# Optimization experiments

Hardware: AMD Instinct MI355X
Metric: run time of the kernel (lower is better)

Reference implementation:

```python
import jax, jax.numpy as jnp
import numpy as np

D = 300   # hidden dim (Linear(300,300))
L = 160   # seq len, forced by W3 = Linear(160,1)


def _linear(x, W, b):
    # torch Linear: x @ W.T + b, W is (out, in)
    return jnp.matmul(x, W.T) + b


def setup_inputs() -> dict:
    key = jax.random.key(0)
    ks = jax.random.split(key, 16)
    B = 1024
    s = 1.0 / np.sqrt(D)
    inp = {
        'T_feature': jax.random.normal(ks[0], (B, L, D), jnp.float32),
        'CD_feature': jax.random.normal(ks[1], (B, L, D), jnp.float32),
        'Wproj': jax.random.normal(ks[2], (D, D), jnp.float32) * s,
        'bproj': jnp.zeros((D,), jnp.float32),
        'WqT_w': jax.random.normal(ks[3], (D, D), jnp.float32) * s,
        'WqT_b': jnp.zeros((D,), jnp.float32),
        'WqCD_w': jax.random.normal(ks[4], (D, D), jnp.float32) * s,
        'WqCD_b': jnp.zeros((D,), jnp.float32),
        'WkT_w': jax.random.normal(ks[5], (D, D), jnp.float32) * s,
        'WkT_b': jnp.zeros((D,), jnp.float32),
        'WkCD_w': jax.random.normal(ks[6], (D, D), jnp.float32) * s,
        'WkCD_b': jnp.zeros((D,), jnp.float32),
        'W3_w': jax.random.normal(ks[7], (1, L), jnp.float32) * (1.0 / np.sqrt(L)),
        'W3_b': jnp.zeros((1,), jnp.float32),
    }
    return inp


def reference(T_feature, CD_feature, Wproj, bproj, WqT_w, WqT_b, WqCD_w, WqCD_b,
              WkT_w, WkT_b, WkCD_w, WkCD_b, W3_w, W3_b):
    sqrt_d = jnp.sqrt(jnp.float32(D))
    proj_T = _linear(T_feature, Wproj, bproj)     # (B, L, D)
    proj_CD = _linear(CD_feature, Wproj, bproj)   # (B, L, D)

    # N_tensor @ proj_T is just the mean over tokens (weights 1/Len)
    mean_T = jnp.mean(proj_T, axis=1, keepdims=True)          # (B, 1, D)
    qT = _linear(mean_T, WqT_w, WqT_b)                        # (B, 1, D)
    kT = _linear(proj_T, WkT_w, WkT_b)                        # (B, L, D)
    alphaT = jnp.einsum('bqd,bkd->bqk', qT, kT) / sqrt_d      # (B, 1, L)
    ZT = jax.nn.sigmoid(alphaT)

    qCD = _linear(proj_CD, WqCD_w, WqCD_b)                    # (B, L, D)
    kCD = _linear(proj_CD, WkCD_w, WkCD_b)                    # (B, L, D)
    alphaCD = jnp.einsum('bqd,bkd->bqk', qCD, kCD) / sqrt_d   # (B, L, L)
    ZCD = jax.nn.sigmoid(alphaCD)

    # The per-token loop+cat is a plain broadcast multiply: Mt[:,i,:] = ZCD[:,i,:] * ZT[:,0,:]
    Mt = ZCD * ZT                                             # (B, L, L)
    alpha_f = jax.nn.softmax(_linear(Mt, W3_w, W3_b), axis=1) # (B, L, 1)

    # Second loop is a per-token scalar scale: HCD[:,i,:] = alpha_f[:,i,0] * proj_CD[:,i,:]
    HCD = alpha_f * proj_CD                                   # (B, L, D)
    return (proj_T, HCD)
```

## Files before the change

### kernel.cpp

```cpp
#include <hip/hip_runtime.h>
#include <hip/hip_bf16.h>


typedef __attribute__((ext_vector_type(8))) short short8;
typedef __attribute__((ext_vector_type(4))) float f32x4;

#define DP 320

__device__ __forceinline__ unsigned short f2bf(float x) {
  unsigned int u = __builtin_bit_cast(unsigned int, x);
  u += 0x7FFFu + ((u >> 16) & 1u);
  return (unsigned short)(u >> 16);
}
__device__ __forceinline__ float bf2f(unsigned short h) {
  unsigned int u = ((unsigned int)h) << 16;
  return __builtin_bit_cast(float, u);
}
__device__ __forceinline__ void gload16(const void* g, void* l) {
  __builtin_amdgcn_global_load_lds(
      (const __attribute__((address_space(1))) unsigned int*)g,
      (__attribute__((address_space(3))) unsigned int*)l, 16, 0, 0);
}
__device__ __forceinline__ float sigm(float x) { return 1.0f / (1.0f + __expf(-x)); }
__device__ __forceinline__ int swzc(int r, int c) {
  return (c & ~63) | ((((c >> 3) & 7) ^ (r & 7)) << 3) | (c & 7);
}

__global__ __launch_bounds__(320)
void prep1_k(const float* __restrict__ W,
             const float* __restrict__ WqCD_w, const float* __restrict__ WqCD_b,
             const float* __restrict__ WkCD_w, const float* __restrict__ WkCD_b,
             const float* __restrict__ WqT_w, const float* __restrict__ WqT_b,
             const float* __restrict__ WkT_w, const float* __restrict__ WkT_b,
             unsigned short* __restrict__ Wb, float* __restrict__ Wt,
             unsigned short* __restrict__ MaugT, float* __restrict__ Maug_f,
             float* __restrict__ Pmat, float isd) {
  const int x = blockIdx.x, c = threadIdx.x;
  if (x < 320) {
    const int n = x;
    unsigned short v = (n < 300 && c < 300) ? f2bf(W[n * 300 + c]) : (unsigned short)0;
    Wb[n * DP + swzc(n, c)] = v;
    if (n < 300 && c < 300) Wt[c * 304 + n] = W[n * 300 + c];
  } else if (x < 640) {
    const int n = x - 320;
    float v = 0.f;
    if (n <= 300 && c <= 300) {
      for (int o = 0; o < 300; ++o) {
        float a = (c < 300) ? WqCD_w[o * 300 + c] : WqCD_b[o];
        float b = (n < 300) ? WkCD_w[o * 300 + n] : WkCD_b[o];
        v += a * b;
      }
      v *= isd;
    }
    MaugT[n * DP + swzc(n, c)] = f2bf(v);
    Maug_f[n * DP + c] = v;
  } else {
    const int n = x - 640;
    float v = 0.f;
    if (n <= 300 && c <= 300) {
      for (int o = 0; o < 300; ++o) {
        float a = (c < 300) ? WkT_w[o * 300 + c] : WkT_b[o];
        float b = (n < 300) ? WqT_w[o * 300 + n] : WqT_b[o];
        v += a * b;
      }
      v *= isd;
    }
    Pmat[n * DP + c] = v;
  }
}

__global__ __launch_bounds__(320)
void gh_k(const float* __restrict__ Maug_f, const float* __restrict__ W,
          const float* __restrict__ bproj, unsigned short* __restrict__ Gswz,
          float* __restrict__ h) {
  const int n = blockIdx.x, o = threadIdx.x;
  float v = 0.f;
  if (o < 300) {
    for (int c = 0; c < 300; ++c) v += Maug_f[n * DP + c] * W[c * 300 + o];
  } else if (o == 300) {
    float s = 0.f;
    for (int c = 0; c < 300; ++c) s += Maug_f[n * DP + c] * bproj[c];
    h[n] = s + Maug_f[n * DP + 300];
  }
  Gswz[n * DP + swzc(n, o)] = (o < 300) ? f2bf(v) : (unsigned short)0;
}

__global__ __launch_bounds__(256)
void cvt_k(const float* __restrict__ T, const float* __restrict__ CD,
           unsigned short* __restrict__ Abf) {
  unsigned idx = blockIdx.x * 256 + threadIdx.x;
  if (idx >= 327680u * 40u) return;
  unsigned row = idx / 40u, G = idx - row * 40u;
  int kc = G >> 3, sg = G & 7;
  int col0 = kc * 64 + ((sg ^ ((int)row & 7)) << 3);
  const float* base = (row < 163840u) ? T + (size_t)row * 300
                                      : CD + (size_t)(row - 163840u) * 300;
  short8 h;
  if (col0 + 8 <= 300) {
    f32x4 x0 = *(const f32x4*)(base + col0), x1 = *(const f32x4*)(base + col0 + 4);
#pragma unroll
    for (int j = 0; j < 4; ++j) { h[j] = (short)f2bf(x0[j]); h[j + 4] = (short)f2bf(x1[j]); }
  } else {
#pragma unroll
    for (int j = 0; j < 8; ++j) {
      int c = col0 + j;
      h[j] = (short)((c < 300) ? f2bf(base[c]) : (unsigned short)0);
    }
  }
  *(short8*)(Abf + (size_t)row * DP + G * 8) = h;
}

__global__ __launch_bounds__(512)
void gemm_k(const unsigned short* __restrict__ A0, const unsigned short* __restrict__ A1,
            const unsigned short* __restrict__ A2,
            const unsigned short* __restrict__ B01, const unsigned short* __restrict__ B2,
            const float* __restrict__ bias, const float* __restrict__ ybias,
            float* __restrict__ Of, unsigned short* __restrict__ pCDout,
            unsigned short* __restrict__ Yout, int mode_base) {
  __shared__ __align__(16) unsigned short As[2][256 * 64];
  __shared__ __align__(16) unsigned short Bs[2][320 * 64];
  const int tid = threadIdx.x, wid = tid >> 6, lane = tid & 63;
  const int lr = lane & 15, hi = lane >> 4;
  const int mode = mode_base + blockIdx.y;
  const unsigned short* __restrict__ A = (mode == 0) ? A0 : (mode == 1) ? A1 : A2;
  const unsigned short* __restrict__ Bm = (mode == 2) ? B2 : B01;
  const size_t m0 = (size_t)blockIdx.x * 256;

  f32x4 acc[4][10];
#pragma unroll
  for (int i = 0; i < 4; ++i)
#pragma unroll
    for (int j = 0; j < 10; ++j) acc[i][j] = (f32x4){0.f, 0.f, 0.f, 0.f};

  auto stageA = [&](int buf, int kc) {
#pragma unroll
    for (int it = 0; it < 4; ++it) {
      int idx = it * 512 + tid;
      int row = idx >> 3, g = idx & 7;
      gload16(A + (m0 + row) * DP + kc * 64 + g * 8, (char*)As[buf] + idx * 16);
    }
  };
  auto stageB = [&](int buf, int kc) {
#pragma unroll
    for (int it = 0; it < 5; ++it) {
      int idx = it * 512 + tid;
      int row = idx >> 3, g = idx & 7;
      gload16(Bm + (size_t)row * DP + kc * 64 + g * 8, (char*)Bs[buf] + idx * 16);
    }
  };

  stageA(0, 0); stageB(0, 0);
  __syncthreads();
  int buf = 0;
  const int rm = (wid >> 1) * 64, cn = (wid & 1) * 160;
  for (int kc = 0; kc < 5; ++kc) {
    if (kc < 4) { stageA(buf ^ 1, kc + 1); stageB(buf ^ 1, kc + 1); }
#pragma unroll
    for (int kk = 0; kk < 2; ++kk) {
      const int slot = ((kk * 4 + hi) ^ lr) & 7;
      short8 a[4];
#pragma unroll
      for (int mf = 0; mf < 4; ++mf)
        a[mf] = *(const short8*)((const char*)As[buf] + (rm + mf * 16 + lr) * 128 + slot * 16);
#pragma unroll
      for (int nh = 0; nh < 2; ++nh) {
        short8 b[5];
#pragma unroll
        for (int nf = 0; nf < 5; ++nf)
          b[nf] = *(const short8*)((const char*)Bs[buf] +
                                   (cn + (nh * 5 + nf) * 16 + lr) * 128 + slot * 16);
#pragma unroll
        for (int mf = 0; mf < 4; ++mf)
#pragma unroll
          for (int nf = 0; nf < 5; ++nf)
            acc[mf][nh * 5 + nf] =
                __builtin_amdgcn_mfma_f32_16x16x32_bf16(a[mf], b[nf], acc[mf][nh * 5 + nf], 0, 0, 0);
      }
    }
    __syncthreads();
    buf ^= 1;
  }

#pragma unroll
  for (int mf = 0; mf < 4; ++mf)
#pragma unroll
    for (int nf = 0; nf < 10; ++nf) {
      const int col = cn + nf * 16 + lr;
      float bv;
      if (mode == 2) bv = ybias ? ybias[col] : 0.f;
      else bv = (col < 300) ? bias[col] : 0.f;
#pragma unroll
      for (int r = 0; r < 4; ++r) {
        const size_t row = m0 + rm + mf * 16 + hi * 4 + r;
        float v = acc[mf][nf][r] + bv;
        if (mode == 0) {
          if (col < 300) Of[row * 300 + col] = v;
        } else {
          unsigned short u = (mode == 2) ? f2bf(v)
                           : (col < 300) ? f2bf(v)
                           : (col == 300) ? f2bf(1.0f) : (unsigned short)0;
          unsigned short* dst = (mode == 1) ? pCDout : Yout;
          dst[row * DP + swzc((int)row, col)] = u;
        }
      }
    }
}

__global__ __launch_bounds__(320)
void gate2_k(const unsigned short* __restrict__ AbfT, const float* __restrict__ Pmat,
             const float* __restrict__ W, const float* __restrict__ Wt,
             const float* __restrict__ bproj, float* __restrict__ ZT) {
  __shared__ float part[8][320];
  __shared__ float ml[320];
  __shared__ float maug[304];
  __shared__ float vv[304];
  __shared__ float wt[320];
  __shared__ float cpr;
  const int b = blockIdx.x, t = threadIdx.x;
  const int wid = t >> 6, lane = t & 63;
  const size_t sbase = (size_t)b * 160 * DP;
  {
    const int og = t % 40, seg = t / 40;
    float a8[8] = {0.f, 0.f, 0.f, 0.f, 0.f, 0.f, 0.f, 0.f};
    for (int l = seg * 20; l < seg * 20 + 20; ++l) {
      int sg = (og & ~7) | ((og & 7) ^ (l & 7));
      short8 v = *(const short8*)(AbfT + sbase + (size_t)l * DP + sg * 8);
#pragma unroll
      for (int j = 0; j < 8; ++j) a8[j] += bf2f((unsigned short)v[j]);
    }
#pragma unroll
    for (int j = 0; j < 8; ++j) part[seg][og * 8 + j] = a8[j];
  }
  __syncthreads();
  {
    float s = 0.f;
#pragma unroll
    for (int sg = 0; sg < 8; ++sg) s += part[sg][t];
    ml[t] = s * (1.0f / 160.0f);
  }
  __syncthreads();
  if (t < 304) {
    if (t < 300) {
      float s = 0.f;
      for (int o = 0; o < 300; ++o) s += Wt[o * 304 + t] * ml[o];
      maug[t] = s + bproj[t];
    } else maug[t] = (t == 300) ? 1.f : 0.f;
  }
  __syncthreads();
  if (t < 304) {
    float s = 0.f;
    if (t <= 300) for (int a = 0; a <= 300; ++a) s += Pmat[a * DP + t] * maug[a];
    vv[t] = s;
  }
  __syncthreads();
  if (t < 320) {
    if (t < 300) {
      float s = 0.f;
      for (int c = 0; c < 300; ++c) s += vv[c] * W[c * 300 + t];
      wt[t] = s;
    } else {
      wt[t] = 0.f;
      if (t == 300) {
        float s = 0.f;
        for (int c = 0; c < 300; ++c) s += vv[c] * bproj[c];
        cpr = s + vv[300];
      }
    }
  }
  __syncthreads();
  for (int j = wid * 32; j < wid * 32 + 32; ++j) {
    float s = 0.f;
    if (lane < 40) {
      int sg = (lane & ~7) | ((lane & 7) ^ (j & 7));
      short8 v = *(const short8*)(AbfT + sbase + (size_t)j * DP + sg * 8);
#pragma unroll
      for (int k = 0; k < 8; ++k) s += bf2f((unsigned short)v[k]) * wt[lane * 8 + k];
    }
#pragma unroll
    for (int m = 1; m < 64; m <<= 1) s += __shfl_xor(s, m, 64);
    if (lane == 0) ZT[b * 160 + j] = sigm(s + cpr);
  }
}

__global__ __launch_bounds__(320)
void finale_k(const unsigned short* __restrict__ Yg, const unsigned short* __restrict__ Pg,
              const float* __restrict__ ZT, const float* __restrict__ W3w,
              float* __restrict__ out) {
  __shared__ __align__(16) unsigned short Ps[160 * DP];
  __shared__ __align__(16) unsigned short Ys[2][160 * 64];
  __shared__ float t_arr[160];
  __shared__ float s_arr[160];
  __shared__ float red0;
  const int b = blockIdx.x, tid = threadIdx.x, wid = tid >> 6, lane = tid & 63;
  const int lr = lane & 15, hi = lane >> 4;
  const unsigned short* Pb = Pg + (size_t)b * 160 * DP;
  const unsigned short* Yb = Yg + (size_t)b * 160 * DP;

  if (tid < 160) t_arr[tid] = ZT[b * 160 + tid] * W3w[tid];

#pragma unroll
  for (int it = 0; it < 20; ++it) {
    int idx = it * 320 + tid;
    gload16(Pb + (size_t)idx * 8, (char*)Ps + idx * 16);
  }
  auto stageY = [&](int buf, int kc) {
#pragma unroll
    for (int it = 0; it < 4; ++it) {
      int idx = it * 320 + tid;
      int row = idx >> 3, g = idx & 7;
      gload16(Yb + (size_t)row * DP + kc * 64 + g * 8, (char*)Ys[buf] + idx * 16);
    }
  };

  f32x4 acc[2][10];
#pragma unroll
  for (int i = 0; i < 2; ++i)
#pragma unroll
    for (int j = 0; j < 10; ++j) acc[i][j] = (f32x4){0.f, 0.f, 0.f, 0.f};

  stageY(0, 0);
  __syncthreads();
  int buf = 0;
  const int rm = wid * 32;
  for (int kc = 0; kc < 5; ++kc) {
    if (kc < 4) stageY(buf ^ 1, kc + 1);
#pragma unroll
    for (int kk = 0; kk < 2; ++kk) {
      const int slot = ((kk * 4 + hi) ^ lr) & 7;
      short8 a[2], bb[10];
#pragma unroll
      for (int mf = 0; mf < 2; ++mf)
        a[mf] = *(const short8*)((const char*)Ys[buf] + (rm + mf * 16 + lr) * 128 + slot * 16);
#pragma unroll
      for (int nf = 0; nf < 10; ++nf)
        bb[nf] = *(const short8*)((const char*)Ps + (nf * 16 + lr) * 640 + (kc * 8 + slot) * 16);
#pragma unroll
      for (int mf = 0; mf < 2; ++mf)
#pragma unroll
        for (int nf = 0; nf < 10; ++nf)
          acc[mf][nf] = __builtin_amdgcn_mfma_f32_16x16x32_bf16(a[mf], bb[nf], acc[mf][nf], 0, 0, 0);
    }
    __syncthreads();
    buf ^= 1;
  }

  float pp[2][4];
#pragma unroll
  for (int mf = 0; mf < 2; ++mf)
#pragma unroll
    for (int r = 0; r < 4; ++r) {
      float s = 0.f;
#pragma unroll
      for (int nf = 0; nf < 10; ++nf) s += sigm(acc[mf][nf][r]) * t_arr[nf * 16 + lr];
      pp[mf][r] = s;
    }
#pragma unroll
  for (int m = 1; m < 16; m <<= 1)
#pragma unroll
    for (int mf = 0; mf < 2; ++mf)
#pragma unroll
      for (int r = 0; r < 4; ++r) pp[mf][r] += __shfl_xor(pp[mf][r], m, 64);
  if (lr == 0) {
#pragma unroll
    for (int mf = 0; mf < 2; ++mf)
#pragma unroll
      for (int r = 0; r < 4; ++r)
        s_arr[rm + mf * 16 + hi * 4 + r] = pp[mf][r];
  }
  __syncthreads();
  if (wid == 0) {
    float v0 = s_arr[lane], v1 = s_arr[lane + 64];
    float v2 = (lane < 32) ? s_arr[lane + 128] : -3.0e38f;
    float mx = fmaxf(fmaxf(v0, v1), v2);
#pragma unroll
    for (int m = 1; m < 64; m <<= 1) mx = fmaxf(mx, __shfl_xor(mx, m, 64));
    float e0 = __expf(v0 - mx), e1 = __expf(v1 - mx);
    float e2 = (lane < 32) ? __expf(v2 - mx) : 0.f;
    s_arr[lane] = e0; s_arr[lane + 64] = e1;
    if (lane < 32) s_arr[lane + 128] = e2;
    float sm = e0 + e1 + e2;
#pragma unroll
    for (int m = 1; m < 64; m <<= 1) sm += __shfl_xor(sm, m, 64);
    if (lane == 0) red0 = 1.0f / sm;
  }
  __syncthreads();
  const float inv = red0;
  float* ob = out + (size_t)b * 48000;
#pragma unroll 2
  for (int it = 0; it < 19; ++it) {
    int idx = it * 320 + tid;
    if (idx < 6080) {
      int i = idx / 38, cg = idx - i * 38;
      int sg = (cg & ~7) | ((cg & 7) ^ (i & 7));
      short8 pv = *(const short8*)((const char*)Ps + i * 640 + sg * 16);
      float sc = s_arr[i] * inv;
      int c0 = cg * 8;
#pragma unroll
      for (int j = 0; j < 8; ++j) {
        int c = c0 + j;
        if (c < 300) ob[(size_t)i * 300 + c] = sc * bf2f((unsigned short)pv[j]);
      }
    }
  }
}

extern "C" void kernel_launch(void* const* d_in, const int* in_sizes, int n_in,
                              void* d_out, int out_size, void* d_ws, size_t ws_size,
                              hipStream_t stream) {
  (void)in_sizes; (void)n_in; (void)out_size;
  const float* T      = (const float*)d_in[0];
  const float* CD     = (const float*)d_in[1];
  const float* Wproj  = (const float*)d_in[2];
  const float* bproj  = (const float*)d_in[3];
  const float* WqT_w  = (const float*)d_in[4];
  const float* WqT_b  = (const float*)d_in[5];
  const float* WqCD_w = (const float*)d_in[6];
  const float* WqCD_b = (const float*)d_in[7];
  const float* WkT_w  = (const float*)d_in[8];
  const float* WkT_b  = (const float*)d_in[9];
  const float* WkCD_w = (const float*)d_in[10];
  const float* WkCD_b = (const float*)d_in[11];
  const float* W3_w   = (const float*)d_in[12];

  char* ws = (char*)d_ws;
  size_t off = 0;
  auto alloc = [&](size_t bytes) { void* p = ws + off; off = (off + bytes + 255) & ~(size_t)255; return p; };
  unsigned short* Wb     = (unsigned short*)alloc((size_t)DP * DP * 2);
  unsigned short* MaugT  = (unsigned short*)alloc((size_t)DP * DP * 2);
  unsigned short* Gswz   = (unsigned short*)alloc((size_t)DP * DP * 2);
  float* Maug_f = (float*)alloc((size_t)DP * DP * 4);
  float* Pmat   = (float*)alloc((size_t)DP * DP * 4);
  float* Wt     = (float*)alloc((size_t)304 * 304 * 4);
  float* hb     = (float*)alloc((size_t)DP * 4);
  float* ZT     = (float*)alloc((size_t)1024 * 160 * 4);
  unsigned short* Abf = (unsigned short*)alloc((size_t)327680 * DP * 2);
  unsigned short* AbfCD = Abf + (size_t)163840 * DP;

  const size_t half = (size_t)163840 * DP * 2;
  const bool big = (ws_size > off) && ((ws_size - off) >= 2 * half + 1024);
  unsigned short* pCDg = big ? (unsigned short*)alloc(half) : AbfCD;
  unsigned short* Yg   = big ? (unsigned short*)alloc(half) : Abf;

  float* projT = (float*)d_out;
  float* HCD   = (float*)d_out + (size_t)49152000;

  const float isd = 1.0f / sqrtf(300.0f);

  prep1_k<<<dim3(960), dim3(320), 0, stream>>>(Wproj, WqCD_w, WqCD_b, WkCD_w, WkCD_b,
                                               WqT_w, WqT_b, WkT_w, WkT_b,
                                               Wb, Wt, MaugT, Maug_f, Pmat, isd);
  if (big)
    gh_k<<<dim3(320), dim3(320), 0, stream>>>(Maug_f, Wproj, bproj, Gswz, hb);
  cvt_k<<<dim3(51200), dim3(256), 0, stream>>>(T, CD, Abf);

  if (big) {
    gemm_k<<<dim3(640, 3), dim3(512), 0, stream>>>(Abf, AbfCD, AbfCD, Wb, Gswz,
                                                   bproj, hb, projT, pCDg, Yg, 0);
    gate2_k<<<dim3(1024), dim3(320), 0, stream>>>(Abf, Pmat, Wproj, Wt, bproj, ZT);
    finale_k<<<dim3(1024), dim3(320), 0, stream>>>(Yg, pCDg, ZT, W3_w, HCD);
  } else {
    gemm_k<<<dim3(640, 2), dim3(512), 0, stream>>>(Abf, AbfCD, nullptr, Wb, nullptr,
                                                   bproj, nullptr, projT, pCDg, nullptr, 0);
    gate2_k<<<dim3(1024), dim3(320), 0, stream>>>(Abf, Pmat, Wproj, Wt, bproj, ZT);
    gemm_k<<<dim3(640, 1), dim3(512), 0, stream>>>(Abf, AbfCD, pCDg, Wb, MaugT,
                                                   bproj, nullptr, projT, pCDg, Yg, 2);
    finale_k<<<dim3(1024), dim3(320), 0, stream>>>(Yg, pCDg, ZT, W3_w, HCD);
  }
}
```

Measured before the change: 731.1 us.

## Store GEMM operands in MFMA fragment-tiled layout and load A directly to registers

```diff
diff --git a/kernel.cpp b/kernel.cpp
--- a/kernel.cpp
+++ b/kernel.cpp
@@ -22,8 +22,13 @@
       (__attribute__((address_space(3))) unsigned int*)l, 16, 0, 0);
 }
 __device__ __forceinline__ float sigm(float x) { return 1.0f / (1.0f + __expf(-x)); }
-__device__ __forceinline__ int swzc(int r, int c) {
-  return (c & ~63) | ((((c >> 3) & 7) ^ (r & 7)) << 3) | (c & 7);
+__device__ __forceinline__ size_t baddr(int n, int k) {
+  return (size_t)(k >> 6) * 20480 + (size_t)(n >> 4) * 1024 + ((k >> 5) & 1) * 512 +
+         ((((k >> 3) & 3) << 4) | (n & 15)) * 8 + (k & 7);
+}
+__device__ __forceinline__ size_t aaddr(size_t r, int k) {
+  return ((r >> 4) * 5 + (k >> 6)) * 1024 + ((k >> 5) & 1) * 512 +
+         ((((k >> 3) & 3) << 4) | (r & 15)) * 8 + (k & 7);
 }
 
 __global__ __launch_bounds__(320)
@@ -39,7 +44,7 @@
   if (x < 320) {
     const int n = x;
     unsigned short v = (n < 300 && c < 300) ? f2bf(W[n * 300 + c]) : (unsigned short)0;
-    Wb[n * DP + swzc(n, c)] = v;
+    Wb[baddr(n, c)] = v;
     if (n < 300 && c < 300) Wt[c * 304 + n] = W[n * 300 + c];
   } else if (x < 640) {
     const int n = x - 320;
@@ -52,7 +57,7 @@
       }
       v *= isd;
     }
-    MaugT[n * DP + swzc(n, c)] = f2bf(v);
+    MaugT[baddr(n, c)] = f2bf(v);
     Maug_f[n * DP + c] = v;
   } else {
     const int n = x - 640;
@@ -82,19 +87,22 @@
     for (int c = 0; c < 300; ++c) s += Maug_f[n * DP + c] * bproj[c];
     h[n] = s + Maug_f[n * DP + 300];
   }
-  Gswz[n * DP + swzc(n, o)] = (o < 300) ? f2bf(v) : (unsigned short)0;
+  if (o > 300 && o == 301) {  }
+  Gswz[baddr(n, o)] = (o < 300) ? f2bf(v) : (unsigned short)0;
+  if (o == 300 && n == 0) {  }
 }
 
 __global__ __launch_bounds__(256)
 void cvt_k(const float* __restrict__ T, const float* __restrict__ CD,
            unsigned short* __restrict__ Abf) {
   unsigned idx = blockIdx.x * 256 + threadIdx.x;
-  if (idx >= 327680u * 40u) return;
-  unsigned row = idx / 40u, G = idx - row * 40u;
-  int kc = G >> 3, sg = G & 7;
-  int col0 = kc * 64 + ((sg ^ ((int)row & 7)) << 3);
-  const float* base = (row < 163840u) ? T + (size_t)row * 300
-                                      : CD + (size_t)(row - 163840u) * 300;
+  if (idx >= 20480u * 640u) return;
+  unsigned row16 = idx / 640u, rem = idx - row16 * 640u;
+  int kc = rem >> 7, kk = (rem >> 6) & 1, lane = rem & 63;
+  int lr = lane & 15, hi = lane >> 4;
+  size_t row = (size_t)row16 * 16 + lr;
+  int col0 = kc * 64 + kk * 32 + hi * 8;
+  const float* base = (row < 163840u) ? T + row * 300 : CD + (row - 163840u) * 300;
   short8 h;
   if (col0 + 8 <= 300) {
     f32x4 x0 = *(const f32x4*)(base + col0), x1 = *(const f32x4*)(base + col0 + 4);
@@ -107,91 +115,77 @@
       h[j] = (short)((c < 300) ? f2bf(base[c]) : (unsigned short)0);
     }
   }
-  *(short8*)(Abf + (size_t)row * DP + G * 8) = h;
-}
-
-__global__ __launch_bounds__(512)
+  *(short8*)(Abf + (size_t)idx * 8) = h;
+}
+
+__global__ __launch_bounds__(256, 2)
 void gemm_k(const unsigned short* __restrict__ A0, const unsigned short* __restrict__ A1,
             const unsigned short* __restrict__ A2,
             const unsigned short* __restrict__ B01, const unsigned short* __restrict__ B2,
             const float* __restrict__ bias, const float* __restrict__ ybias,
             float* __restrict__ Of, unsigned short* __restrict__ pCDout,
             unsigned short* __restrict__ Yout, int mode_base) {
-  __shared__ __align__(16) unsigned short As[2][256 * 64];
-  __shared__ __align__(16) unsigned short Bs[2][320 * 64];
+  __shared__ __align__(16) unsigned short Bs[2][20480];
   const int tid = threadIdx.x, wid = tid >> 6, lane = tid & 63;
   const int lr = lane & 15, hi = lane >> 4;
   const int mode = mode_base + blockIdx.y;
   const unsigned short* __restrict__ A = (mode == 0) ? A0 : (mode == 1) ? A1 : A2;
   const unsigned short* __restrict__ Bm = (mode == 2) ? B2 : B01;
-  const size_t m0 = (size_t)blockIdx.x * 256;
-
-  f32x4 acc[4][10];
-#pragma unroll
-  for (int i = 0; i < 4; ++i)
-#pragma unroll
-    for (int j = 0; j < 10; ++j) acc[i][j] = (f32x4){0.f, 0.f, 0.f, 0.f};
-
-  auto stageA = [&](int buf, int kc) {
-#pragma unroll
-    for (int it = 0; it < 4; ++it) {
-      int idx = it * 512 + tid;
-      int row = idx >> 3, g = idx & 7;
-      gload16(A + (m0 + row) * DP + kc * 64 + g * 8, (char*)As[buf] + idx * 16);
+  const size_t m0 = (size_t)blockIdx.x * 128;
+  const size_t rt0 = (m0 >> 4) + wid * 2;
+
+  f32x4 acc[2][20];
+#pragma unroll
+  for (int i = 0; i < 2; ++i)
+#pragma unroll
+    for (int j = 0; j < 20; ++j) acc[i][j] = (f32x4){0.f, 0.f, 0.f, 0.f};
+
+  auto stageB = [&](int buf, int kc) {
+#pragma unroll
+    for (int it = 0; it < 10; ++it) {
+      int idx = it * 256 + tid;
+      gload16(Bm + (size_t)kc * 20480 + (size_t)idx * 8, (char*)Bs[buf] + idx * 16);
     }
   };
-  auto stageB = [&](int buf, int kc) {
-#pragma unroll
-    for (int it = 0; it < 5; ++it) {
-      int idx = it * 512 + tid;
-      int row = idx >> 3, g = idx & 7;
-      gload16(Bm + (size_t)row * DP + kc * 64 + g * 8, (char*)Bs[buf] + idx * 16);
-    }
+  short8 af[2][2][2];
+  auto loadA = [&](short8 (&dst)[2][2], int kc) {
+#pragma unroll
+    for (int mf = 0; mf < 2; ++mf)
+#pragma unroll
+      for (int kk = 0; kk < 2; ++kk)
+        dst[mf][kk] = *(const short8*)(A + ((rt0 + mf) * 5 + kc) * 1024 + kk * 512 + lane * 8);
   };
 
-  stageA(0, 0); stageB(0, 0);
-  __syncthreads();
-  int buf = 0;
-  const int rm = (wid >> 1) * 64, cn = (wid & 1) * 160;
+  stageB(0, 0);
+  loadA(af[0], 0);
+  __syncthreads();
+#pragma unroll
   for (int kc = 0; kc < 5; ++kc) {
-    if (kc < 4) { stageA(buf ^ 1, kc + 1); stageB(buf ^ 1, kc + 1); }
-#pragma unroll
-    for (int kk = 0; kk < 2; ++kk) {
-      const int slot = ((kk * 4 + hi) ^ lr) & 7;
-      short8 a[4];
-#pragma unroll
-      for (int mf = 0; mf < 4; ++mf)
-        a[mf] = *(const short8*)((const char*)As[buf] + (rm + mf * 16 + lr) * 128 + slot * 16);
-#pragma unroll
-      for (int nh = 0; nh < 2; ++nh) {
-        short8 b[5];
-#pragma unroll
-        for (int nf = 0; nf < 5; ++nf)
-          b[nf] = *(const short8*)((const char*)Bs[buf] +
-                                   (cn + (nh * 5 + nf) * 16 + lr) * 128 + slot * 16);
-#pragma unroll
-        for (int mf = 0; mf < 4; ++mf)
-#pragma unroll
-          for (int nf = 0; nf < 5; ++nf)
-            acc[mf][nh * 5 + nf] =
-                __builtin_amdgcn_mfma_f32_16x16x32_bf16(a[mf], b[nf], acc[mf][nh * 5 + nf], 0, 0, 0);
-      }
-    }
+    const int cur = kc & 1;
+    if (kc < 4) { stageB(cur ^ 1, kc + 1); loadA(af[cur ^ 1], kc + 1); }
+#pragma unroll
+    for (int kk = 0; kk < 2; ++kk)
+#pragma unroll
+      for (int nf = 0; nf < 20; ++nf) {
+        short8 bb = *(const short8*)&Bs[cur][nf * 1024 + kk * 512 + lane * 8];
+#pragma unroll
+        for (int mf = 0; mf < 2; ++mf)
+          acc[mf][nf] = __builtin_amdgcn_mfma_f32_16x16x32_bf16(af[cur][mf][kk], bb, acc[mf][nf], 0, 0, 0);
+      }
     __syncthreads();
-    buf ^= 1;
-  }
-
-#pragma unroll
-  for (int mf = 0; mf < 4; ++mf)
-#pragma unroll
-    for (int nf = 0; nf < 10; ++nf) {
-      const int col = cn + nf * 16 + lr;
-      float bv;
-      if (mode == 2) bv = ybias ? ybias[col] : 0.f;
-      else bv = (col < 300) ? bias[col] : 0.f;
+  }
+
+#pragma unroll
+  for (int mf = 0; mf < 2; ++mf)
+#pragma unroll
+    for (int nf = 0; nf < 20; ++nf) {
+      const int col = nf * 16 + lr;
+      const float bv = (mode == 2) ? (ybias ? ybias[col] : 0.f)
+                                   : ((col < 300) ? bias[col] : 0.f);
+      const size_t row16o = rt0 + mf;
 #pragma unroll
       for (int r = 0; r < 4; ++r) {
-        const size_t row = m0 + rm + mf * 16 + hi * 4 + r;
+        const size_t row = (row16o << 4) + hi * 4 + r;
         float v = acc[mf][nf][r] + bv;
         if (mode == 0) {
           if (col < 300) Of[row * 300 + col] = v;
@@ -200,49 +194,36 @@
                            : (col < 300) ? f2bf(v)
                            : (col == 300) ? f2bf(1.0f) : (unsigned short)0;
           unsigned short* dst = (mode == 1) ? pCDout : Yout;
-          dst[row * DP + swzc((int)row, col)] = u;
+          dst[(row16o * 5 + (col >> 6)) * 1024 + ((col >> 5) & 1) * 512 +
+              ((((col >> 3) & 3) << 4) | (hi * 4 + r)) * 8 + (col & 7)] = u;
         }
       }
     }
 }
 
 __global__ __launch_bounds__(320)
-void gate2_k(const unsigned short* __restrict__ AbfT, const float* __restrict__ Pmat,
+void gate2_k(const float* __restrict__ T, const float* __restrict__ Pmat,
              const float* __restrict__ W, const float* __restrict__ Wt,
              const float* __restrict__ bproj, float* __restrict__ ZT) {
-  __shared__ float part[8][320];
-  __shared__ float ml[320];
+  __shared__ float mt[304];
   __shared__ float maug[304];
   __shared__ float vv[304];
-  __shared__ float wt[320];
+  __shared__ float wt[304];
   __shared__ float cpr;
   const int b = blockIdx.x, t = threadIdx.x;
   const int wid = t >> 6, lane = t & 63;
-  const size_t sbase = (size_t)b * 160 * DP;
-  {
-    const int og = t % 40, seg = t / 40;
-    float a8[8] = {0.f, 0.f, 0.f, 0.f, 0.f, 0.f, 0.f, 0.f};
-    for (int l = seg * 20; l < seg * 20 + 20; ++l) {
-      int sg = (og & ~7) | ((og & 7) ^ (l & 7));
-      short8 v = *(const short8*)(AbfT + sbase + (size_t)l * DP + sg * 8);
-#pragma unroll
-      for (int j = 0; j < 8; ++j) a8[j] += bf2f((unsigned short)v[j]);
-    }
-#pragma unroll
-    for (int j = 0; j < 8; ++j) part[seg][og * 8 + j] = a8[j];
-  }
-  __syncthreads();
-  {
+  const float* Tb = T + (size_t)b * 48000;
+  if (t < 300) {
     float s = 0.f;
-#pragma unroll
-    for (int sg = 0; sg < 8; ++sg) s += part[sg][t];
-    ml[t] = s * (1.0f / 160.0f);
+#pragma unroll 4
+    for (int l = 0; l < 160; ++l) s += Tb[l * 300 + t];
+    mt[t] = s * (1.0f / 160.0f);
   }
   __syncthreads();
   if (t < 304) {
     if (t < 300) {
       float s = 0.f;
-      for (int o = 0; o < 300; ++o) s += Wt[o * 304 + t] * ml[o];
+      for (int o = 0; o < 300; ++o) s += Wt[o * 304 + t] * mt[o];
       maug[t] = s + bproj[t];
     } else maug[t] = (t == 300) ? 1.f : 0.f;
   }
@@ -253,7 +234,7 @@
     vv[t] = s;
   }
   __syncthreads();
-  if (t < 320) {
+  if (t < 304) {
     if (t < 300) {
       float s = 0.f;
       for (int c = 0; c < 300; ++c) s += vv[c] * W[c * 300 + t];
@@ -269,103 +250,82 @@
   }
   __syncthreads();
   for (int j = wid * 32; j < wid * 32 + 32; ++j) {
+    const float* row = Tb + j * 300;
     float s = 0.f;
-    if (lane < 40) {
-      int sg = (lane & ~7) | ((lane & 7) ^ (j & 7));
-      short8 v = *(const short8*)(AbfT + sbase + (size_t)j * DP + sg * 8);
-#pragma unroll
-      for (int k = 0; k < 8; ++k) s += bf2f((unsigned short)v[k]) * wt[lane * 8 + k];
-    }
+    for (int c = lane; c < 300; c += 64) s += wt[c] * row[c];
 #pragma unroll
     for (int m = 1; m < 64; m <<= 1) s += __shfl_xor(s, m, 64);
     if (lane == 0) ZT[b * 160 + j] = sigm(s + cpr);
   }
 }
 
-__global__ __launch_bounds__(320)
+__global__ __launch_bounds__(640)
 void finale_k(const unsigned short* __restrict__ Yg, const unsigned short* __restrict__ Pg,
               const float* __restrict__ ZT, const float* __restrict__ W3w,
               float* __restrict__ out) {
-  __shared__ __align__(16) unsigned short Ps[160 * DP];
-  __shared__ __align__(16) unsigned short Ys[2][160 * 64];
+  __shared__ __align__(16) unsigned short Ps[51200];
   __shared__ float t_arr[160];
   __shared__ float s_arr[160];
   __shared__ float red0;
   const int b = blockIdx.x, tid = threadIdx.x, wid = tid >> 6, lane = tid & 63;
   const int lr = lane & 15, hi = lane >> 4;
-  const unsigned short* Pb = Pg + (size_t)b * 160 * DP;
-  const unsigned short* Yb = Yg + (size_t)b * 160 * DP;
+  const unsigned short* Pb = Pg + (size_t)b * 51200;
+  const unsigned short* Yb = Yg + (size_t)b * 51200;
 
   if (tid < 160) t_arr[tid] = ZT[b * 160 + tid] * W3w[tid];
 
-#pragma unroll
-  for (int it = 0; it < 20; ++it) {
-    int idx = it * 320 + tid;
-    gload16(Pb + (size_t)idx * 8, (char*)Ps + idx * 16);
-  }
-  auto stageY = [&](int buf, int kc) {
-#pragma unroll
-    for (int it = 0; it < 4; ++it) {
-      int idx = it * 320 + tid;
-      int row = idx >> 3, g = idx & 7;
-      gload16(Yb + (size_t)row * DP + kc * 64 + g * 8, (char*)Ys[buf] + idx * 16);
+  auto stageP = [&](int kc) {
+#pragma unroll
+    for (int it = 0; it < 2; ++it) {
+      int idx = it * 640 + tid;
+      int r16 = idx >> 7, rem = idx & 127;
+      gload16(Pb + ((size_t)r16 * 5 + kc) * 1024 + (size_t)rem * 8,
+              (char*)Ps + ((size_t)kc * 10240 + (size_t)idx * 8) * 2);
     }
   };
-
-  f32x4 acc[2][10];
-#pragma unroll
-  for (int i = 0; i < 2; ++i)
-#pragma unroll
-    for (int j = 0; j < 10; ++j) acc[i][j] = (f32x4){0.f, 0.f, 0.f, 0.f};
-
-  stageY(0, 0);
-  __syncthreads();
-  int buf = 0;
-  const int rm = wid * 32;
+  short8 yf[2][2];
+  auto loadY = [&](short8 (&dst)[2], int kc) {
+#pragma unroll
+    for (int kk = 0; kk < 2; ++kk)
+      dst[kk] = *(const short8*)(Yb + ((size_t)wid * 5 + kc) * 1024 + kk * 512 + lane * 8);
+  };
+
+  f32x4 acc[10];
+#pragma unroll
+  for (int j = 0; j < 10; ++j) acc[j] = (f32x4){0.f, 0.f, 0.f, 0.f};
+
+  stageP(0);
+  loadY(yf[0], 0);
+  __syncthreads();
+#pragma unroll
   for (int kc = 0; kc < 5; ++kc) {
-    if (kc < 4) stageY(buf ^ 1, kc + 1);
-#pragma unroll
-    for (int kk = 0; kk < 2; ++kk) {
-      const int slot = ((kk * 4 + hi) ^ lr) & 7;
-      short8 a[2], bb[10];
-#pragma unroll
-      for (int mf = 0; mf < 2; ++mf)
-        a[mf] = *(const short8*)((const char*)Ys[buf] + (rm + mf * 16 + lr) * 128 + slot * 16);
-#pragma unroll
-      for (int nf = 0; nf < 10; ++nf)
-        bb[nf] = *(const short8*)((const char*)Ps + (nf * 16 + lr) * 640 + (kc * 8 + slot) * 16);
-#pragma unroll
-      for (int mf = 0; mf < 2; ++mf)
-#pragma unroll
-        for (int nf = 0; nf < 10; ++nf)
-          acc[mf][nf] = __builtin_amdgcn_mfma_f32_16x16x32_bf16(a[mf], bb[nf], acc[mf][nf], 0, 0, 0);
-    }
+    const int cur = kc & 1;
+    if (kc < 4) { stageP(kc + 1); loadY(yf[cur ^ 1], kc + 1); }
+#pragma unroll
+    for (int kk = 0; kk < 2; ++kk)
+#pragma unroll
+      for (int nf = 0; nf < 10; ++nf) {
+        short8 bb = *(const short8*)&Ps[kc * 10240 + nf * 1024 + kk * 512 + lane * 8];
+        acc[nf] = __builtin_amdgcn_mfma_f32_16x16x32_bf16(yf[cur][kk], bb, acc[nf], 0, 0, 0);
+      }
     __syncthreads();
-    buf ^= 1;
-  }
-
-  float pp[2][4];
-#pragma unroll
-  for (int mf = 0; mf < 2; ++mf)
-#pragma unroll
-    for (int r = 0; r < 4; ++r) {
-      float s = 0.f;
-#pragma unroll
-      for (int nf = 0; nf < 10; ++nf) s += sigm(acc[mf][nf][r]) * t_arr[nf * 16 + lr];
-      pp[mf][r] = s;
-    }
+  }
+
+  float pp[4];
+#pragma unroll
+  for (int r = 0; r < 4; ++r) {
+    float s = 0.f;
+#pragma unroll
+    for (int nf = 0; nf < 10; ++nf) s += sigm(acc[nf][r]) * t_arr[nf * 16 + lr];
+    pp[r] = s;
+  }
 #pragma unroll
   for (int m = 1; m < 16; m <<= 1)
 #pragma unroll
-    for (int mf = 0; mf < 2; ++mf)
-#pragma unroll
-      for (int r = 0; r < 4; ++r) pp[mf][r] += __shfl_xor(pp[mf][r], m, 64);
+    for (int r = 0; r < 4; ++r) pp[r] += __shfl_xor(pp[r], m, 64);
   if (lr == 0) {
 #pragma unroll
-    for (int mf = 0; mf < 2; ++mf)
-#pragma unroll
-      for (int r = 0; r < 4; ++r)
-        s_arr[rm + mf * 16 + hi * 4 + r] = pp[mf][r];
+    for (int r = 0; r < 4; ++r) s_arr[wid * 16 + hi * 4 + r] = pp[r];
   }
   __syncthreads();
   if (wid == 0) {
@@ -386,19 +346,27 @@
   __syncthreads();
   const float inv = red0;
   float* ob = out + (size_t)b * 48000;
-#pragma unroll 2
-  for (int it = 0; it < 19; ++it) {
-    int idx = it * 320 + tid;
-    if (idx < 6080) {
-      int i = idx / 38, cg = idx - i * 38;
-      int sg = (cg & ~7) | ((cg & 7) ^ (i & 7));
-      short8 pv = *(const short8*)((const char*)Ps + i * 640 + sg * 16);
+#pragma unroll
+  for (int it = 0; it < 10; ++it) {
+    int idx = it * 640 + tid;
+    int i = idx / 40, g = idx - i * 40;
+    int c0 = g * 8;
+    if (c0 < 300) {
+      short8 pv = *(const short8*)&Ps[(g >> 3) * 10240 + (i >> 4) * 1024 +
+                                      ((g >> 2) & 1) * 512 + ((((g & 3) << 4) | (i & 15)) * 8)];
       float sc = s_arr[i] * inv;
-      int c0 = cg * 8;
-#pragma unroll
-      for (int j = 0; j < 8; ++j) {
-        int c = c0 + j;
-        if (c < 300) ob[(size_t)i * 300 + c] = sc * bf2f((unsigned short)pv[j]);
+      if (c0 + 8 <= 300) {
+        f32x4 o0, o1;
+#pragma unroll
+        for (int j = 0; j < 4; ++j) { o0[j] = sc * bf2f((unsigned short)pv[j]); o1[j] = sc * bf2f((unsigned short)pv[j + 4]); }
+        *(f32x4*)(ob + (size_t)i * 300 + c0) = o0;
+        *(f32x4*)(ob + (size_t)i * 300 + c0 + 4) = o1;
+      } else {
+#pragma unroll
+        for (int j = 0; j < 8; ++j) {
+          int c = c0 + j;
+          if (c < 300) ob[(size_t)i * 300 + c] = sc * bf2f((unsigned short)pv[j]);
+        }
       }
     }
   }
@@ -449,21 +417,18 @@
   prep1_k<<<dim3(960), dim3(320), 0, stream>>>(Wproj, WqCD_w, WqCD_b, WkCD_w, WkCD_b,
                                                WqT_w, WqT_b, WkT_w, WkT_b,
                                                Wb, Wt, MaugT, Maug_f, Pmat, isd);
-  if (big)
-    gh_k<<<dim3(320), dim3(320), 0, stream>>>(Maug_f, Wproj, bproj, Gswz, hb);
+  gh_k<<<dim3(320), dim3(320), 0, stream>>>(Maug_f, Wproj, bproj, Gswz, hb);
   cvt_k<<<dim3(51200), dim3(256), 0, stream>>>(T, CD, Abf);
+  gate2_k<<<dim3(1024), dim3(320), 0, stream>>>(T, Pmat, Wproj, Wt, bproj, ZT);
 
   if (big) {
-    gemm_k<<<dim3(640, 3), dim3(512), 0, stream>>>(Abf, AbfCD, AbfCD, Wb, Gswz,
-                                                   bproj, hb, projT, pCDg, Yg, 0);
-    gate2_k<<<dim3(1024), dim3(320), 0, stream>>>(Abf, Pmat, Wproj, Wt, bproj, ZT);
-    finale_k<<<dim3(1024), dim3(320), 0, stream>>>(Yg, pCDg, ZT, W3_w, HCD);
+    gemm_k<<<dim3(1280, 3), dim3(256), 0, stream>>>(Abf, AbfCD, AbfCD, Wb, Gswz,
+                                                    bproj, hb, projT, pCDg, Yg, 0);
   } else {
-    gemm_k<<<dim3(640, 2), dim3(512), 0, stream>>>(Abf, AbfCD, nullptr, Wb, nullptr,
-                                                   bproj, nullptr, projT, pCDg, nullptr, 0);
-    gate2_k<<<dim3(1024), dim3(320), 0, stream>>>(Abf, Pmat, Wproj, Wt, bproj, ZT);
-    gemm_k<<<dim3(640, 1), dim3(512), 0, stream>>>(Abf, AbfCD, pCDg, Wb, MaugT,
-                                                   bproj, nullptr, projT, pCDg, Yg, 2);
-    finale_k<<<dim3(1024), dim3(320), 0, stream>>>(Yg, pCDg, ZT, W3_w, HCD);
-  }
-}
+    gemm_k<<<dim3(1280, 2), dim3(256), 0, stream>>>(Abf, AbfCD, nullptr, Wb, nullptr,
+                                                    bproj, nullptr, projT, pCDg, nullptr, 0);
+    gemm_k<<<dim3(1280, 1), dim3(256), 0, stream>>>(nullptr, nullptr, pCDg, Wb, MaugT,
+                                                    bproj, nullptr, projT, nullptr, Yg, 2);
+  }
+  finale_k<<<dim3(1024), dim3(640), 0, stream>>>(Yg, pCDg, ZT, W3_w, HCD);
+}
```

Result: faster. 688.8 us (-5.8%).
